# Kernel optimization log

Hardware: AMD Instinct MI355X
Metric: run time of the kernel (lower is better)

Reference implementation:

```python
import jax, jax.numpy as jnp
import numpy as np

T, M, HW = 16, 256, 1024
D_MODEL, D_K, H = 512, 512, 8
HEAD = D_K // H
SIGMA = 0.5
EPS = 1e-6

def layernorm_nobias(x, gamma):
    mu = jnp.mean(x, axis=-1, keepdims=True)
    var = jnp.mean((x - mu) ** 2, axis=-1, keepdims=True)
    return (x - mu) * jax.lax.rsqrt(var + EPS) * gamma

def setup_inputs() -> dict:
    key = jax.random.key(0)
    ks = jax.random.split(key, 11)
    s = 0.02
    return {
        "updated_track_tokens": jax.random.normal(ks[0], (T, M, D_MODEL), jnp.float32),
        "tracks": jax.random.uniform(ks[1], (T, M, 2), jnp.float32) * 32.0,
        "feature_positions": jax.random.uniform(ks[2], (HW, 2), jnp.float32) * 32.0,
        "feature_pos_embeddings": jax.random.normal(ks[3], (T, HW, D_MODEL), jnp.float32),
        "track_pos_embeddings": jax.random.normal(ks[4], (T, M, D_MODEL), jnp.float32),
        "W_q": jax.random.normal(ks[5], (D_K, D_MODEL), jnp.float32) * s,
        "W_k": jax.random.normal(ks[6], (D_K, D_MODEL), jnp.float32) * s,
        "W_v": jax.random.normal(ks[7], (D_MODEL, D_MODEL), jnp.float32) * s,
        "W_out": jax.random.normal(ks[8], (D_MODEL, D_MODEL), jnp.float32) * s,
        "q_gamma": jnp.ones((D_K,), jnp.float32),
        "k_gamma": jnp.ones((D_K,), jnp.float32),
    }

def reference(updated_track_tokens, tracks, feature_positions, feature_pos_embeddings,
              track_pos_embeddings, W_q, W_k, W_v, W_out, q_gamma, k_gamma):
    # Projections (torch Linear: x @ W.T)
    Q = feature_pos_embeddings @ W_q.T       # [T, HW, D_K]
    K = track_pos_embeddings @ W_k.T         # [T, M, D_K]
    V = updated_track_tokens @ W_v.T         # [T, M, D_MODEL]
    # QK LayerNorm (no bias) over full d_k, before head split
    Q = layernorm_nobias(Q, q_gamma)
    K = layernorm_nobias(K, k_gamma)
    Qh = Q.reshape(T, HW, H, HEAD).transpose(0, 2, 1, 3)          # [T,H,HW,hd]
    Kh = K.reshape(T, M, H, HEAD).transpose(0, 2, 1, 3)           # [T,H,M,hd]
    Vh = V.reshape(T, M, H, D_MODEL // H).transpose(0, 2, 1, 3)   # [T,H,M,dv]
    scores = jnp.einsum('thqd,thkd->thqk', Qh, Kh) / np.float32(np.sqrt(HEAD))
    # Vectorized spatial bias: squared euclidean distance feat->track per t
    diff = feature_positions[None, :, None, :] - tracks[:, None, :, :]  # [T,HW,M,2]
    d2 = jnp.sum(diff * diff, axis=-1)                                  # [T,HW,M]
    bias = -d2 / (2.0 * SIGMA ** 2)
    scores = scores + bias[:, None, :, :]                               # broadcast heads
    attn = jax.nn.softmax(scores, axis=-1)
    upd = jnp.einsum('thqk,thkd->thqd', attn, Vh)                       # [T,H,HW,dv]
    upd = upd.transpose(0, 2, 1, 3).reshape(T, HW, D_MODEL)
    return upd @ W_out.T
```

## Files before the change

kernel.cpp:

```cpp
#include <hip/hip_runtime.h>

#define T_    16
#define M_    256
#define HW_   1024
#define DM    512
#define H_    8
#define HEAD_ 64
#define LOG2E 1.4426950408889634f

typedef __attribute__((ext_vector_type(8))) short short8;
typedef __attribute__((ext_vector_type(4))) float f32x4;

__device__ __forceinline__ unsigned cvtpk(float lo, float hi) {
    unsigned r;
    asm("v_cvt_pk_bf16_f32 %0, %1, %2" : "=v"(r) : "v"(lo), "v"(hi));
    return r;
}

__device__ __forceinline__ void gload16(const void* g, void* l) {
    __builtin_amdgcn_global_load_lds(
        (const __attribute__((address_space(1))) void*)g,
        (__attribute__((address_space(3))) void*)l, 16, 0, 0);
}

__global__ __launch_bounds__(256) void cvtall(const float* __restrict__ fpe,
                                              const float* __restrict__ tpe,
                                              const float* __restrict__ utt,
                                              const float* __restrict__ Wq,
                                              const float* __restrict__ Wk,
                                              const float* __restrict__ Wv,
                                              const float* __restrict__ Wo,
                                              unsigned short* __restrict__ Fb,
                                              unsigned short* __restrict__ Tb,
                                              unsigned short* __restrict__ Ub0,
                                              unsigned short* __restrict__ Wbf) {
    size_t e = (size_t)(blockIdx.x * 256 + threadIdx.x) * 8;
    const float* s;
    unsigned short* d;
    if (e < 8388608)        { s = fpe + e;              d = Fb  + e; }
    else if (e < 10485760)  { s = tpe + (e - 8388608);  d = Tb  + (e - 8388608); }
    else if (e < 12582912)  { s = utt + (e - 10485760); d = Ub0 + (e - 10485760); }
    else if (e < 12845056)  { s = Wq  + (e - 12582912); d = Wbf + (e - 12582912 + 0); }
    else if (e < 13107200)  { s = Wk  + (e - 12845056); d = Wbf + (e - 12845056 + 262144); }
    else if (e < 13369344)  { s = Wv  + (e - 13107200); d = Wbf + (e - 13107200 + 524288); }
    else                    { s = Wo  + (e - 13369344); d = Wbf + (e - 13369344 + 786432); }
    float4 a = *reinterpret_cast<const float4*>(s);
    float4 b = *reinterpret_cast<const float4*>(s + 4);
    uint4 v = make_uint4(cvtpk(a.x, a.y), cvtpk(a.z, a.w),
                         cvtpk(b.x, b.y), cvtpk(b.z, b.w));
    *reinterpret_cast<uint4*>(d) = v;
}

__global__ __launch_bounds__(256) void proj3(const unsigned short* __restrict__ Fb,
                                             const unsigned short* __restrict__ Tb,
                                             const unsigned short* __restrict__ Ub0,
                                             const unsigned short* __restrict__ Wbf,
                                             float* __restrict__ Qf,
                                             float* __restrict__ Kf,
                                             float* __restrict__ Vf) {
    __shared__ __align__(16) unsigned char smem[32768];
    unsigned char* As = smem;
    unsigned char* Bs = smem + 16384;

    const int b  = blockIdx.x;
    const int x  = b & 7;
    const int cp = (b >> 3) & 3;
    const int m  = b >> 5;
    const int p  = x * 24 + m;
    const unsigned short *X, *W;
    float* C;
    int r0;
    if (p < 128)      { X = Fb;  W = Wbf;          C = Qf; r0 = p * 128; }
    else if (p < 160) { X = Tb;  W = Wbf + 262144; C = Kf; r0 = (p - 128) * 128; }
    else              { X = Ub0; W = Wbf + 524288; C = Vf; r0 = (p - 160) * 128; }
    const int c0 = cp * 128;

    const int tid = threadIdx.x;
    const int l  = tid & 63;
    const int wid = tid >> 6;
    const int wr = wid >> 1, wc = wid & 1;
    const int g = l >> 4;
    const int c = l & 15;

    f32x4 acc[4][4] = {};

    for (int k0 = 0; k0 < DM; k0 += 64) {
        #pragma unroll
        for (int i = 0; i < 4; ++i) {
            int idx = tid + i * 256;
            int row = idx >> 3, jj = idx & 7;
            int j = jj ^ (row & 7);
            gload16(X + (size_t)(r0 + row) * DM + k0 + j * 8, As + idx * 16);
            gload16(W + (size_t)(c0 + row) * DM + k0 + j * 8, Bs + idx * 16);
        }
        __syncthreads();

        #pragma unroll
        for (int ks = 0; ks < 2; ++ks) {
            short8 af[4], bfr[4];
            #pragma unroll
            for (int mm = 0; mm < 4; ++mm) {
                int rq = wr * 64 + mm * 16 + c;
                af[mm] = *reinterpret_cast<short8*>(
                    As + ((rq * 128 + ks * 64 + g * 16) ^ ((rq & 7) << 4)));
            }
            #pragma unroll
            for (int n = 0; n < 4; ++n) {
                int rn = wc * 64 + n * 16 + c;
                bfr[n] = *reinterpret_cast<short8*>(
                    Bs + ((rn * 128 + ks * 64 + g * 16) ^ ((rn & 7) << 4)));
            }
            #pragma unroll
            for (int mm = 0; mm < 4; ++mm)
                #pragma unroll
                for (int n = 0; n < 4; ++n)
                    acc[mm][n] = __builtin_amdgcn_mfma_f32_16x16x32_bf16(
                        af[mm], bfr[n], acc[mm][n], 0, 0, 0);
        }
        __syncthreads();
    }

    #pragma unroll
    for (int mm = 0; mm < 4; ++mm)
        #pragma unroll
        for (int n = 0; n < 4; ++n)
            #pragma unroll
            for (int r = 0; r < 4; ++r)
                C[(size_t)(r0 + wr * 64 + mm * 16 + g * 4 + r) * DM +
                  c0 + wc * 64 + n * 16 + c] = acc[mm][n][r];
}

__global__ __launch_bounds__(256) void gemm_bb(const unsigned short* __restrict__ X,
                                               const unsigned short* __restrict__ W,
                                               float* __restrict__ C) {
    __shared__ __align__(16) unsigned char smem[32768];
    unsigned char* As = smem;
    unsigned char* Bs = smem + 16384;

    const int b  = blockIdx.x;
    const int x  = b & 7;
    const int cp = (b >> 3) & 3;
    const int m  = b >> 5;
    const int p  = x * 16 + m;
    const int r0 = p * 128;
    const int c0 = cp * 128;

    const int tid = threadIdx.x;
    const int l  = tid & 63;
    const int wid = tid >> 6;
    const int wr = wid >> 1, wc = wid & 1;
    const int g = l >> 4;
    const int c = l & 15;

    f32x4 acc[4][4] = {};

    for (int k0 = 0; k0 < DM; k0 += 64) {
        #pragma unroll
        for (int i = 0; i < 4; ++i) {
            int idx = tid + i * 256;
            int row = idx >> 3, jj = idx & 7;
            int j = jj ^ (row & 7);
            gload16(X + (size_t)(r0 + row) * DM + k0 + j * 8, As + idx * 16);
            gload16(W + (size_t)(c0 + row) * DM + k0 + j * 8, Bs + idx * 16);
        }
        __syncthreads();

        #pragma unroll
        for (int ks = 0; ks < 2; ++ks) {
            short8 af[4], bfr[4];
            #pragma unroll
            for (int mm = 0; mm < 4; ++mm) {
                int rq = wr * 64 + mm * 16 + c;
                af[mm] = *reinterpret_cast<short8*>(
                    As + ((rq * 128 + ks * 64 + g * 16) ^ ((rq & 7) << 4)));
            }
            #pragma unroll
            for (int n = 0; n < 4; ++n) {
                int rn = wc * 64 + n * 16 + c;
                bfr[n] = *reinterpret_cast<short8*>(
                    Bs + ((rn * 128 + ks * 64 + g * 16) ^ ((rn & 7) << 4)));
            }
            #pragma unroll
            for (int mm = 0; mm < 4; ++mm)
                #pragma unroll
                for (int n = 0; n < 4; ++n)
                    acc[mm][n] = __builtin_amdgcn_mfma_f32_16x16x32_bf16(
                        af[mm], bfr[n], acc[mm][n], 0, 0, 0);
        }
        __syncthreads();
    }

    #pragma unroll
    for (int mm = 0; mm < 4; ++mm)
        #pragma unroll
        for (int n = 0; n < 4; ++n)
            #pragma unroll
            for (int r = 0; r < 4; ++r)
                C[(size_t)(r0 + wr * 64 + mm * 16 + g * 4 + r) * DM +
                  c0 + wc * 64 + n * 16 + c] = acc[mm][n][r];
}

__global__ __launch_bounds__(256) void normpack(const float* __restrict__ Qf,
                                                const float* __restrict__ Kf,
                                                const float* __restrict__ Vf,
                                                const float* __restrict__ qg,
                                                const float* __restrict__ kg,
                                                unsigned short* __restrict__ Qbf,
                                                unsigned short* __restrict__ Kbf,
                                                unsigned short* __restrict__ Vt) {
    __shared__ float tile[64][65];
    const int bid = blockIdx.x;
    const int tid = threadIdx.x;

    if (bid < 5120) {
        const float* X; const float* gamma; unsigned short* Y; int rowbase; float sc;
        if (bid < 4096) { X = Qf; gamma = qg; Y = Qbf; rowbase = bid * 4; sc = 0.125f * LOG2E; }
        else            { X = Kf; gamma = kg; Y = Kbf; rowbase = (bid - 4096) * 4; sc = 1.0f; }

        const int wave = tid / 64;
        const int lane = tid % 64;
        const int row  = rowbase + wave;

        float4 v0 = *reinterpret_cast<const float4*>(&X[(size_t)row * DM + lane * 8]);
        float4 v1 = *reinterpret_cast<const float4*>(&X[(size_t)row * DM + lane * 8 + 4]);
        float x[8] = {v0.x, v0.y, v0.z, v0.w, v1.x, v1.y, v1.z, v1.w};

        float s = 0.f;
        #pragma unroll
        for (int i = 0; i < 8; ++i) s += x[i];
        #pragma unroll
        for (int m = 1; m < 64; m <<= 1) s += __shfl_xor(s, m, 64);
        const float mu = s * (1.0f / 512.0f);

        float vs = 0.f;
        #pragma unroll
        for (int i = 0; i < 8; ++i) { float d = x[i] - mu; vs += d * d; }
        #pragma unroll
        for (int m = 1; m < 64; m <<= 1) vs += __shfl_xor(vs, m, 64);
        const float rs = rsqrtf(vs * (1.0f / 512.0f) + 1e-6f) * sc;

        float4 g0 = *reinterpret_cast<const float4*>(&gamma[lane * 8]);
        float4 g1 = *reinterpret_cast<const float4*>(&gamma[lane * 8 + 4]);
        float gv[8] = {g0.x, g0.y, g0.z, g0.w, g1.x, g1.y, g1.z, g1.w};

        float y[8];
        #pragma unroll
        for (int i = 0; i < 8; ++i) y[i] = (x[i] - mu) * rs * gv[i];
        uint4 o = make_uint4(cvtpk(y[0], y[1]), cvtpk(y[2], y[3]),
                             cvtpk(y[4], y[5]), cvtpk(y[6], y[7]));
        *reinterpret_cast<uint4*>(&Y[(size_t)row * DM + lane * 8]) = o;
    } else {
        const int b2 = bid - 5120;
        const int dt = b2 & 7, kt = (b2 >> 3) & 3, t = b2 >> 5;

        #pragma unroll
        for (int i = 0; i < 4; ++i) {
            int idx = tid + i * 256;
            int r = idx >> 4, c4 = idx & 15;
            float4 v = *reinterpret_cast<const float4*>(
                &Vf[(size_t)(t * M_ + kt * 64 + r) * DM + dt * 64 + c4 * 4]);
            tile[r][c4 * 4 + 0] = v.x;
            tile[r][c4 * 4 + 1] = v.y;
            tile[r][c4 * 4 + 2] = v.z;
            tile[r][c4 * 4 + 3] = v.w;
        }
        __syncthreads();
        #pragma unroll
        for (int i = 0; i < 4; ++i) {
            int idx = tid + i * 256;
            int r = idx >> 4, c4 = idx & 15;
            uint2 o = make_uint2(cvtpk(tile[c4 * 4 + 0][r], tile[c4 * 4 + 1][r]),
                                 cvtpk(tile[c4 * 4 + 2][r], tile[c4 * 4 + 3][r]));
            *reinterpret_cast<uint2*>(
                &Vt[((size_t)t * DM + dt * 64 + r) * M_ + kt * 64 + c4 * 4]) = o;
        }
    }
}

__global__ __launch_bounds__(256, 4) void attn_mfma(const unsigned short* __restrict__ Qbf,
                                                    const unsigned short* __restrict__ Kbf,
                                                    const unsigned short* __restrict__ VtG,
                                                    const float* __restrict__ tracks,
                                                    const float* __restrict__ fpos,
                                                    unsigned short* __restrict__ Ubf) {
    const int b   = blockIdx.x;
    const int xcd = b & 7;
    const int bi  = b >> 3;
    const int qt  = bi & 15;
    const int pp  = xcd + (bi >> 4) * 8;
    const int t   = pp >> 3;
    const int h   = pp & 7;
    const int q0  = qt * 64;
    const int tid = threadIdx.x;

    __shared__ __align__(16) unsigned char smem[32768 + 3072 + 512];
    unsigned char* KV = smem;
    float* tx4 = (float*)(smem + 32768);
    float* ty4 = (float*)(smem + 32768 + 1024);
    float* tz2 = (float*)(smem + 32768 + 2048);
    float* fps = (float*)(smem + 32768 + 3072);

    const int l  = tid & 63;
    const int wq = tid >> 6;
    const int g  = l >> 4;
    const int c  = l & 15;

    const unsigned short* qrow =
        Qbf + (size_t)(t * HW_ + q0 + wq * 16 + c) * DM + h * HEAD_;
    short8 bQ0 = *reinterpret_cast<const short8*>(qrow + g * 8);
    short8 bQ1 = *reinterpret_cast<const short8*>(qrow + 32 + g * 8);

    #pragma unroll
    for (int it = 0; it < 8; ++it) {
        int idx = tid + it * 256;
        int row = idx >> 3, jj = idx & 7;
        int j = jj ^ (row & 7);
        gload16(Kbf + (size_t)(t * M_ + row) * DM + h * HEAD_ + j * 8, KV + idx * 16);
    }
    {
        float2 tk = *reinterpret_cast<const float2*>(&tracks[t * 512 + tid * 2]);
        tx4[tid] = tk.x * (4.0f * LOG2E);
        ty4[tid] = tk.y * (4.0f * LOG2E);
        tz2[tid] = -2.0f * LOG2E * (tk.x * tk.x + tk.y * tk.y);
    }
    if (tid < 128) fps[tid] = fpos[q0 * 2 + tid];
    __syncthreads();

    f32x4 acc[16];
    __builtin_amdgcn_s_setprio(1);
    #pragma unroll
    for (int n = 0; n < 16; ++n) {
        int rk = n * 16 + c;
        short8 a0 = *reinterpret_cast<short8*>(KV + ((rk * 128 + g * 16) ^ ((rk & 7) << 4)));
        short8 a1 = *reinterpret_cast<short8*>(KV + ((rk * 128 + 64 + g * 16) ^ ((rk & 7) << 4)));
        f32x4 z = {0.f, 0.f, 0.f, 0.f};
        z = __builtin_amdgcn_mfma_f32_16x16x32_bf16(a0, bQ0, z, 0, 0, 0);
        z = __builtin_amdgcn_mfma_f32_16x16x32_bf16(a1, bQ1, z, 0, 0, 0);
        acc[n] = z;
    }
    __builtin_amdgcn_s_setprio(0);

    const float fx = fps[(wq * 16 + c) * 2];
    const float fy = fps[(wq * 16 + c) * 2 + 1];
    #pragma unroll
    for (int n = 0; n < 16; ++n) {
        float4 x4 = *reinterpret_cast<float4*>(&tx4[n * 16 + g * 4]);
        float4 y4 = *reinterpret_cast<float4*>(&ty4[n * 16 + g * 4]);
        float4 z4 = *reinterpret_cast<float4*>(&tz2[n * 16 + g * 4]);
        acc[n][0] += fmaf(fx, x4.x, fmaf(fy, y4.x, z4.x));
        acc[n][1] += fmaf(fx, x4.y, fmaf(fy, y4.y, z4.y));
        acc[n][2] += fmaf(fx, x4.z, fmaf(fy, y4.z, z4.z));
        acc[n][3] += fmaf(fx, x4.w, fmaf(fy, y4.w, z4.w));
    }

    float vr[16];
    #pragma unroll
    for (int n = 0; n < 16; ++n)
        vr[n] = fmaxf(fmaxf(acc[n][0], acc[n][1]), fmaxf(acc[n][2], acc[n][3]));
    #pragma unroll
    for (int s = 8; s >= 1; s >>= 1)
        #pragma unroll
        for (int n = 0; n < 8; ++n)
            if (n < s) vr[n] = fmaxf(vr[n], vr[n + s]);
    float mx = vr[0];
    mx = fmaxf(mx, __shfl_xor(mx, 16, 64));
    mx = fmaxf(mx, __shfl_xor(mx, 32, 64));

    #pragma unroll
    for (int n = 0; n < 16; ++n)
        #pragma unroll
        for (int r = 0; r < 4; ++r)
            acc[n][r] = exp2f(acc[n][r] - mx);

    unsigned pk[16][2];
    #pragma unroll
    for (int n = 0; n < 16; ++n) {
        pk[n][0] = cvtpk(acc[n][0], acc[n][1]);
        pk[n][1] = cvtpk(acc[n][2], acc[n][3]);
    }

    __syncthreads();

    #pragma unroll
    for (int it = 0; it < 8; ++it) {
        int idx = tid + it * 256;
        int row = idx >> 5, kcc = idx & 31;
        int kc = kcc ^ (row & 7);
        gload16(VtG + ((size_t)t * DM + h * HEAD_ + row) * M_ + kc * 8, KV + idx * 16);
    }

    #pragma unroll
    for (int n = 0; n < 16; ++n)
        vr[n] = (acc[n][0] + acc[n][1]) + (acc[n][2] + acc[n][3]);
    #pragma unroll
    for (int s = 8; s >= 1; s >>= 1)
        #pragma unroll
        for (int n = 0; n < 8; ++n)
            if (n < s) vr[n] += vr[n + s];
    float sum = vr[0];
    sum += __shfl_xor(sum, 16, 64);
    sum += __shfl_xor(sum, 32, 64);
    const float inv = 1.0f / sum;

    float invr[4];
    #pragma unroll
    for (int r = 0; r < 4; ++r)
        invr[r] = __shfl(inv, (l & 48) | ((l >> 2) & 12) | r, 64);

    __syncthreads();

    f32x4 o[4] = {{0.f,0.f,0.f,0.f},{0.f,0.f,0.f,0.f},{0.f,0.f,0.f,0.f},{0.f,0.f,0.f,0.f}};
    __builtin_amdgcn_s_setprio(1);
    #pragma unroll
    for (int ks = 0; ks < 8; ++ks) {
        unsigned wb[4];
        #pragma unroll
        for (int wt = 0; wt < 4; ++wt) {
            int src = ((l & 16) << 1) + (wt >> 1) * 16 + c;
            unsigned ve = (unsigned)__shfl((int)pk[2 * ks][wt & 1], src, 64);
            unsigned vo = (unsigned)__shfl((int)pk[2 * ks + 1][wt & 1], src, 64);
            wb[wt] = (g < 2) ? ve : vo;
        }
        uint4 uu = make_uint4(wb[0], wb[1], wb[2], wb[3]);
        short8 aP = *reinterpret_cast<short8*>(&uu);
        #pragma unroll
        for (int nv = 0; nv < 4; ++nv) {
            int rv = nv * 16 + c;
            short8 bV = *reinterpret_cast<short8*>(
                KV + ((rv * 512 + ks * 64 + g * 16) ^ ((rv & 7) << 4)));
            o[nv] = __builtin_amdgcn_mfma_f32_16x16x32_bf16(aP, bV, o[nv], 0, 0, 0);
        }
    }
    __builtin_amdgcn_s_setprio(0);

    #pragma unroll
    for (int nv = 0; nv < 4; ++nv)
        #pragma unroll
        for (int r = 0; r < 4; ++r) {
            float x = o[nv][r] * invr[r];
            Ubf[(size_t)(t * HW_ + q0 + wq * 16 + g * 4 + r) * DM +
                h * HEAD_ + nv * 16 + c] = (unsigned short)cvtpk(x, x);
        }
}

extern "C" void kernel_launch(void* const* d_in, const int* in_sizes, int n_in,
                              void* d_out, int out_size, void* d_ws, size_t ws_size,
                              hipStream_t stream) {
    const float* utt    = (const float*)d_in[0];
    const float* tracks = (const float*)d_in[1];
    const float* fpos   = (const float*)d_in[2];
    const float* fpe    = (const float*)d_in[3];
    const float* tpe    = (const float*)d_in[4];
    const float* Wq     = (const float*)d_in[5];
    const float* Wk     = (const float*)d_in[6];
    const float* Wv     = (const float*)d_in[7];
    const float* Wo     = (const float*)d_in[8];
    const float* qgamma = (const float*)d_in[9];
    const float* kgamma = (const float*)d_in[10];
    float* out = (float*)d_out;

    char* ws = (char*)d_ws;
    float*          Qf  = (float*)(ws);
    float*          Kf  = (float*)(ws + 33554432);
    float*          Vf  = (float*)(ws + 41943040);
    unsigned short* Qbf = (unsigned short*)(ws + 50331648);
    unsigned short* Kbf = (unsigned short*)(ws + 67108864);
    unsigned short* Vt  = (unsigned short*)(ws + 71303168);
    unsigned short* Wbf = (unsigned short*)(ws + 75497472);
    unsigned short* Fb  = Qbf;
    unsigned short* Tb  = Kbf;
    unsigned short* Ub0 = Vt;
    unsigned short* Ubf = (unsigned short*)(ws);

    cvtall<<<6656, 256, 0, stream>>>(fpe, tpe, utt, Wq, Wk, Wv, Wo, Fb, Tb, Ub0, Wbf);

    proj3<<<768, 256, 0, stream>>>(Fb, Tb, Ub0, Wbf, Qf, Kf, Vf);

    normpack<<<5632, 256, 0, stream>>>(Qf, Kf, Vf, qgamma, kgamma, Qbf, Kbf, Vt);

    attn_mfma<<<2048, 256, 0, stream>>>(Qbf, Kbf, Vt, tracks, fpos, Ubf);

    gemm_bb<<<512, 256, 0, stream>>>(Ubf, Wbf + 786432, out);
}
```

Measured before the change: 105.4 us.

## Fuse activation fp32-to-bf16 conversion into projection GEMM and emit bf16 projections

The separate pass that converts the activations to bf16 is removed. The projection GEMM now loads fp32 activations directly, converts them in registers and stores them into swizzled LDS, while only the weights are still pre-converted. The projection outputs are written as bf16 instead of fp32, which roughly halves the intermediate traffic read by the layernorm/transpose pass. In exchange, the A-operand loads no longer use asynchronous global-to-LDS transfers and read twice the bytes per element through registers. LayerNorm statistics are also computed from bf16-rounded projections, so precision drops slightly.

```diff
diff --git a/kernel.cpp b/kernel.cpp
--- a/kernel.cpp
+++ b/kernel.cpp
@@ -17,47 +17,38 @@
     return r;
 }
 
+__device__ __forceinline__ float b2f(unsigned short u) {
+    return __uint_as_float(((unsigned)u) << 16);
+}
+
 __device__ __forceinline__ void gload16(const void* g, void* l) {
     __builtin_amdgcn_global_load_lds(
         (const __attribute__((address_space(1))) void*)g,
         (__attribute__((address_space(3))) void*)l, 16, 0, 0);
 }
 
-__global__ __launch_bounds__(256) void cvtall(const float* __restrict__ fpe,
-                                              const float* __restrict__ tpe,
-                                              const float* __restrict__ utt,
-                                              const float* __restrict__ Wq,
-                                              const float* __restrict__ Wk,
-                                              const float* __restrict__ Wv,
-                                              const float* __restrict__ Wo,
-                                              unsigned short* __restrict__ Fb,
-                                              unsigned short* __restrict__ Tb,
-                                              unsigned short* __restrict__ Ub0,
-                                              unsigned short* __restrict__ Wbf) {
-    size_t e = (size_t)(blockIdx.x * 256 + threadIdx.x) * 8;
-    const float* s;
-    unsigned short* d;
-    if (e < 8388608)        { s = fpe + e;              d = Fb  + e; }
-    else if (e < 10485760)  { s = tpe + (e - 8388608);  d = Tb  + (e - 8388608); }
-    else if (e < 12582912)  { s = utt + (e - 10485760); d = Ub0 + (e - 10485760); }
-    else if (e < 12845056)  { s = Wq  + (e - 12582912); d = Wbf + (e - 12582912 + 0); }
-    else if (e < 13107200)  { s = Wk  + (e - 12845056); d = Wbf + (e - 12845056 + 262144); }
-    else if (e < 13369344)  { s = Wv  + (e - 13107200); d = Wbf + (e - 13107200 + 524288); }
-    else                    { s = Wo  + (e - 13369344); d = Wbf + (e - 13369344 + 786432); }
-    float4 a = *reinterpret_cast<const float4*>(s);
-    float4 b = *reinterpret_cast<const float4*>(s + 4);
+__global__ __launch_bounds__(256) void cvtw(const float* __restrict__ W0,
+                                            const float* __restrict__ W1,
+                                            const float* __restrict__ W2,
+                                            const float* __restrict__ W3,
+                                            unsigned short* __restrict__ O) {
+    const int y = blockIdx.y;
+    const float* src = (y == 0) ? W0 : (y == 1) ? W1 : (y == 2) ? W2 : W3;
+    const int base = (blockIdx.x * 256 + threadIdx.x) * 8;
+    float4 a = *reinterpret_cast<const float4*>(src + base);
+    float4 b = *reinterpret_cast<const float4*>(src + base + 4);
     uint4 v = make_uint4(cvtpk(a.x, a.y), cvtpk(a.z, a.w),
                          cvtpk(b.x, b.y), cvtpk(b.z, b.w));
-    *reinterpret_cast<uint4*>(d) = v;
-}
-
-__global__ __launch_bounds__(256) void proj3(const unsigned short* __restrict__ Fb,
-                                             const unsigned short* __restrict__ Tb,
-                                             const unsigned short* __restrict__ Ub0,
+    *reinterpret_cast<uint4*>(O + (size_t)y * 262144 + base) = v;
+}
+
+__global__ __launch_bounds__(256) void proj3(const float* __restrict__ fpe,
+                                             const float* __restrict__ tpe,
+                                             const float* __restrict__ utt,
                                              const unsigned short* __restrict__ Wbf,
-                                             float* __restrict__ Qf,
-                                             float* __restrict__ Kf,
-                                             float* __restrict__ Vf) {
+                                             unsigned short* __restrict__ Qb,
+                                             unsigned short* __restrict__ Kb,
+                                             unsigned short* __restrict__ Vb) {
     __shared__ __align__(16) unsigned char smem[32768];
     unsigned char* As = smem;
     unsigned char* Bs = smem + 16384;
@@ -67,12 +58,13 @@
     const int cp = (b >> 3) & 3;
     const int m  = b >> 5;
     const int p  = x * 24 + m;
-    const unsigned short *X, *W;
-    float* C;
+    const float* X;
+    const unsigned short* W;
+    unsigned short* C;
     int r0;
-    if (p < 128)      { X = Fb;  W = Wbf;          C = Qf; r0 = p * 128; }
-    else if (p < 160) { X = Tb;  W = Wbf + 262144; C = Kf; r0 = (p - 128) * 128; }
-    else              { X = Ub0; W = Wbf + 524288; C = Vf; r0 = (p - 160) * 128; }
+    if (p < 128)      { X = fpe; W = Wbf;          C = Qb; r0 = p * 128; }
+    else if (p < 160) { X = tpe; W = Wbf + 262144; C = Kb; r0 = (p - 128) * 128; }
+    else              { X = utt; W = Wbf + 524288; C = Vb; r0 = (p - 160) * 128; }
     const int c0 = cp * 128;
 
     const int tid = threadIdx.x;
@@ -88,10 +80,20 @@
         #pragma unroll
         for (int i = 0; i < 4; ++i) {
             int idx = tid + i * 256;
-            int row = idx >> 3, jj = idx & 7;
-            int j = jj ^ (row & 7);
-            gload16(X + (size_t)(r0 + row) * DM + k0 + j * 8, As + idx * 16);
-            gload16(W + (size_t)(c0 + row) * DM + k0 + j * 8, Bs + idx * 16);
+            int row = idx >> 3, dc = idx & 7;
+            {
+                const float* s = X + (size_t)(r0 + row) * DM + k0 + dc * 8;
+                float4 a = *reinterpret_cast<const float4*>(s);
+                float4 bb = *reinterpret_cast<const float4*>(s + 4);
+                uint4 v = make_uint4(cvtpk(a.x, a.y), cvtpk(a.z, a.w),
+                                     cvtpk(bb.x, bb.y), cvtpk(bb.z, bb.w));
+                *reinterpret_cast<uint4*>(
+                    As + ((row * 128 + dc * 16) ^ ((row & 7) << 4))) = v;
+            }
+            {
+                int j = dc ^ (row & 7);
+                gload16(W + (size_t)(c0 + row) * DM + k0 + j * 8, Bs + idx * 16);
+            }
         }
         __syncthreads();
 
@@ -127,7 +129,8 @@
             #pragma unroll
             for (int r = 0; r < 4; ++r)
                 C[(size_t)(r0 + wr * 64 + mm * 16 + g * 4 + r) * DM +
-                  c0 + wc * 64 + n * 16 + c] = acc[mm][n][r];
+                  c0 + wc * 64 + n * 16 + c] =
+                    (unsigned short)cvtpk(acc[mm][n][r], acc[mm][n][r]);
 }
 
 __global__ __launch_bounds__(256) void gemm_bb(const unsigned short* __restrict__ X,
@@ -200,30 +203,32 @@
                   c0 + wc * 64 + n * 16 + c] = acc[mm][n][r];
 }
 
-__global__ __launch_bounds__(256) void normpack(const float* __restrict__ Qf,
-                                                const float* __restrict__ Kf,
-                                                const float* __restrict__ Vf,
+__global__ __launch_bounds__(256) void normpack(const unsigned short* __restrict__ Qb,
+                                                const unsigned short* __restrict__ Kb,
+                                                const unsigned short* __restrict__ Vb,
                                                 const float* __restrict__ qg,
                                                 const float* __restrict__ kg,
                                                 unsigned short* __restrict__ Qbf,
                                                 unsigned short* __restrict__ Kbf,
                                                 unsigned short* __restrict__ Vt) {
-    __shared__ float tile[64][65];
+    __shared__ unsigned short vtile[64][68];
     const int bid = blockIdx.x;
     const int tid = threadIdx.x;
 
     if (bid < 5120) {
-        const float* X; const float* gamma; unsigned short* Y; int rowbase; float sc;
-        if (bid < 4096) { X = Qf; gamma = qg; Y = Qbf; rowbase = bid * 4; sc = 0.125f * LOG2E; }
-        else            { X = Kf; gamma = kg; Y = Kbf; rowbase = (bid - 4096) * 4; sc = 1.0f; }
+        const unsigned short* X; const float* gamma; unsigned short* Y;
+        int rowbase; float sc;
+        if (bid < 4096) { X = Qb; gamma = qg; Y = Qbf; rowbase = bid * 4; sc = 0.125f * LOG2E; }
+        else            { X = Kb; gamma = kg; Y = Kbf; rowbase = (bid - 4096) * 4; sc = 1.0f; }
 
         const int wave = tid / 64;
         const int lane = tid % 64;
         const int row  = rowbase + wave;
 
-        float4 v0 = *reinterpret_cast<const float4*>(&X[(size_t)row * DM + lane * 8]);
-        float4 v1 = *reinterpret_cast<const float4*>(&X[(size_t)row * DM + lane * 8 + 4]);
-        float x[8] = {v0.x, v0.y, v0.z, v0.w, v1.x, v1.y, v1.z, v1.w};
+        short8 xv = *reinterpret_cast<const short8*>(&X[(size_t)row * DM + lane * 8]);
+        float x[8];
+        #pragma unroll
+        for (int i = 0; i < 8; ++i) x[i] = b2f((unsigned short)xv[i]);
 
         float s = 0.f;
         #pragma unroll
@@ -257,20 +262,18 @@
         for (int i = 0; i < 4; ++i) {
             int idx = tid + i * 256;
             int r = idx >> 4, c4 = idx & 15;
-            float4 v = *reinterpret_cast<const float4*>(
-                &Vf[(size_t)(t * M_ + kt * 64 + r) * DM + dt * 64 + c4 * 4]);
-            tile[r][c4 * 4 + 0] = v.x;
-            tile[r][c4 * 4 + 1] = v.y;
-            tile[r][c4 * 4 + 2] = v.z;
-            tile[r][c4 * 4 + 3] = v.w;
+            uint2 v = *reinterpret_cast<const uint2*>(
+                &Vb[(size_t)(t * M_ + kt * 64 + r) * DM + dt * 64 + c4 * 4]);
+            *reinterpret_cast<uint2*>(&vtile[r][c4 * 4]) = v;
         }
         __syncthreads();
         #pragma unroll
         for (int i = 0; i < 4; ++i) {
             int idx = tid + i * 256;
             int r = idx >> 4, c4 = idx & 15;
-            uint2 o = make_uint2(cvtpk(tile[c4 * 4 + 0][r], tile[c4 * 4 + 1][r]),
-                                 cvtpk(tile[c4 * 4 + 2][r], tile[c4 * 4 + 3][r]));
+            unsigned a0 = vtile[c4 * 4 + 0][r], a1 = vtile[c4 * 4 + 1][r];
+            unsigned a2 = vtile[c4 * 4 + 2][r], a3 = vtile[c4 * 4 + 3][r];
+            uint2 o = make_uint2(a0 | (a1 << 16), a2 | (a3 << 16));
             *reinterpret_cast<uint2*>(
                 &Vt[((size_t)t * DM + dt * 64 + r) * M_ + kt * 64 + c4 * 4]) = o;
         }
@@ -437,9 +440,9 @@
     for (int nv = 0; nv < 4; ++nv)
         #pragma unroll
         for (int r = 0; r < 4; ++r) {
-            float x = o[nv][r] * invr[r];
+            float xo = o[nv][r] * invr[r];
             Ubf[(size_t)(t * HW_ + q0 + wq * 16 + g * 4 + r) * DM +
-                h * HEAD_ + nv * 16 + c] = (unsigned short)cvtpk(x, x);
+                h * HEAD_ + nv * 16 + c] = (unsigned short)cvtpk(xo, xo);
         }
 }
 
@@ -460,23 +463,20 @@
     float* out = (float*)d_out;
 
     char* ws = (char*)d_ws;
-    float*          Qf  = (float*)(ws);
-    float*          Kf  = (float*)(ws + 33554432);
-    float*          Vf  = (float*)(ws + 41943040);
+    unsigned short* Qb  = (unsigned short*)(ws);
+    unsigned short* Kb  = (unsigned short*)(ws + 16777216);
+    unsigned short* Vb  = (unsigned short*)(ws + 20971520);
     unsigned short* Qbf = (unsigned short*)(ws + 50331648);
     unsigned short* Kbf = (unsigned short*)(ws + 67108864);
     unsigned short* Vt  = (unsigned short*)(ws + 71303168);
     unsigned short* Wbf = (unsigned short*)(ws + 75497472);
-    unsigned short* Fb  = Qbf;
-    unsigned short* Tb  = Kbf;
-    unsigned short* Ub0 = Vt;
     unsigned short* Ubf = (unsigned short*)(ws);
 
-    cvtall<<<6656, 256, 0, stream>>>(fpe, tpe, utt, Wq, Wk, Wv, Wo, Fb, Tb, Ub0, Wbf);
-
-    proj3<<<768, 256, 0, stream>>>(Fb, Tb, Ub0, Wbf, Qf, Kf, Vf);
-
-    normpack<<<5632, 256, 0, stream>>>(Qf, Kf, Vf, qgamma, kgamma, Qbf, Kbf, Vt);
+    cvtw<<<dim3(128, 4), 256, 0, stream>>>(Wq, Wk, Wv, Wo, Wbf);
+
+    proj3<<<768, 256, 0, stream>>>(fpe, tpe, utt, Wbf, Qb, Kb, Vb);
+
+    normpack<<<5632, 256, 0, stream>>>(Qb, Kb, Vb, qgamma, kgamma, Qbf, Kbf, Vt);
 
     attn_mfma<<<2048, 256, 0, stream>>>(Qbf, Kbf, Vt, tracks, fpos, Ubf);
 
```

New measurement: 108.0 us. 1.02x slower.
